# Optimization experiments

Hardware: AMD Instinct MI355X
Metric: run time of the kernel (lower is better)

The kernel has to match this reference:

```python
import jax, jax.numpy as jnp
import numpy as np

SMU_ALPHA = 0.25
SMU_MU = 1.0e6  # repo's act.SMU default: large mu -> smooth leaky-relu (max(x, alpha*x))

def smu(x):
    a = SMU_ALPHA
    return 0.5 * ((1.0 + a) * x + (1.0 - a) * x * jax.lax.erf(SMU_MU * (1.0 - a) * x))

def setup_inputs() -> dict:
    key = jax.random.key(0)
    ks = jax.random.split(key, 6)
    B, N, D = 8, 4096, 1024
    xavier = float(np.sqrt(6.0 / (D + D)))
    def lin_w(k):
        return jax.random.uniform(k, (D, D), jnp.float32, -xavier, xavier)
    return {
        "x": jax.random.normal(ks[0], (B, N, D), jnp.float32),
        "Wvr": lin_w(ks[1]), "bvr": jnp.zeros((D,), jnp.float32),
        "Wvi": lin_w(ks[2]), "bvi": jnp.zeros((D,), jnp.float32),
        "Wk": lin_w(ks[3]), "bk": jnp.zeros((D,), jnp.float32),
        "Wq": lin_w(ks[4]), "bq": jnp.zeros((D,), jnp.float32),
    }

def reference(x, Wvr, bvr, Wvi, bvi, Wk, bk, Wq, bq):
    # real input: real and imag branches both see x
    value_real = jnp.einsum('bnd,ed->bne', x, Wvr) + bvr
    value_imag = jnp.einsum('bnd,ed->bne', x, Wvi) + bvi
    # GLU: v_real * tanh(softplus(v_imag)); dropout disabled (p=0)
    value = value_real * jnp.tanh(jax.nn.softplus(value_imag))
    key_ = jnp.einsum('bnd,ed->bne', x, Wk) + bk
    query = jnp.einsum('bnd,ed->bne', x, Wq) + bq
    # L2 normalize along the sequence dim (dim=1)
    key_n = key_ / (jnp.linalg.norm(key_, axis=1, keepdims=True) + 1e-5)
    query_n = query / (jnp.linalg.norm(query, axis=1, keepdims=True) + 1e-5)
    feature_attn = smu(jnp.einsum('bnd,bne->bde', key_n, query_n))  # [B, D, D]
    return jnp.einsum('bnd,bde->bne', value, feature_attn)
```

## Files before the change

### kernel.cpp

```cpp
#include <hip/hip_runtime.h>
#include <math.h>

typedef __bf16 bf16x8 __attribute__((ext_vector_type(8)));
typedef float f32x4 __attribute__((ext_vector_type(4)));

#define MTOT 32768
#define DD   1024
#define NSEQ 4096
#define BB   8

__device__ __forceinline__ void async16(const void* gp, void* lp) {
  __builtin_amdgcn_global_load_lds(
      (__attribute__((address_space(1))) void*)(const_cast<void*>(gp)),
      (__attribute__((address_space(3))) void*)(lp), 16, 0, 0);
}

__device__ __forceinline__ unsigned short f2bf(float f) {
  union { float f; unsigned int u; } v; v.f = f;
  unsigned int r = v.u + 0x7fffu + ((v.u >> 16) & 1u);
  return (unsigned short)(r >> 16);
}
__device__ __forceinline__ float bf2f(unsigned short u) {
  union { unsigned int u; float f; } v; v.u = ((unsigned int)u) << 16; return v.f;
}

__device__ __forceinline__ unsigned lds_off(void* p) {
  return (unsigned)(unsigned long long)
      (__attribute__((address_space(3))) void*)p;
}
#define DSRI(dst, base, off) \
  asm volatile("ds_read_b128 %0, %1 offset:" #off : "=v"(dst) : "v"(base))

#define MFMA_ __builtin_amdgcn_mfma_f32_16x16x32_bf16

__global__ void cvt_bf16(const float* __restrict__ in, unsigned short* __restrict__ out, int n) {
  int i = (blockIdx.x * blockDim.x + threadIdx.x) * 8;
  if (i >= n) return;
  float4 a = *(const float4*)(in + i);
  float4 b = *(const float4*)(in + i + 4);
  ushort4 o0, o1;
  o0.x = f2bf(a.x); o0.y = f2bf(a.y); o0.z = f2bf(a.z); o0.w = f2bf(a.w);
  o1.x = f2bf(b.x); o1.y = f2bf(b.y); o1.z = f2bf(b.z); o1.w = f2bf(b.w);
  *(ushort4*)(out + i) = o0;
  *(ushort4*)(out + i + 4) = o1;
}

__global__ void cvt_w(const float* __restrict__ w0, const float* __restrict__ w1,
                      const float* __restrict__ w2, const float* __restrict__ w3,
                      unsigned short* __restrict__ out) {
  int z = blockIdx.y;
  const float* in = (z == 0) ? w0 : (z == 1) ? w1 : (z == 2) ? w2 : w3;
  int i = (blockIdx.x * blockDim.x + threadIdx.x) * 8;
  float4 a = *(const float4*)(in + i);
  float4 b = *(const float4*)(in + i + 4);
  ushort4 o0, o1;
  o0.x = f2bf(a.x); o0.y = f2bf(a.y); o0.z = f2bf(a.z); o0.w = f2bf(a.w);
  o1.x = f2bf(b.x); o1.y = f2bf(b.y); o1.z = f2bf(b.z); o1.w = f2bf(b.w);
  unsigned short* o = out + (size_t)z * DD * DD;
  *(ushort4*)(o + i) = o0;
  *(ushort4*)(o + i + 4) = o1;
}

template<int LDG>
__device__ __forceinline__ void stage_half(const unsigned short* __restrict__ g,
                                           int row0, int k0,
                                           unsigned short* lds, int tid) {
#pragma unroll
  for (int l = 0; l < 2; ++l) {
    int u = l * 512 + tid;
    int r = u >> 3;
    int sl = (u & 7) ^ (r & 7);
    async16(g + (size_t)(row0 + r) * LDG + k0 + sl * 8, (char*)lds + u * 16);
  }
}

__global__ __launch_bounds__(512, 2) void proj_all(
    const unsigned short* __restrict__ xb,
    const unsigned short* __restrict__ Wb,
    const float* __restrict__ bvr, const float* __restrict__ bvi,
    const float* __restrict__ bk,  const float* __restrict__ bq,
    unsigned short* __restrict__ oVr, unsigned short* __restrict__ oVi,
    unsigned short* __restrict__ Kt,  unsigned short* __restrict__ Qt,
    float* __restrict__ rnacc) {
  __shared__ __align__(16) unsigned short smem[65536];

  const int bx = blockIdx.x;
  const int swz = (bx & 7) * 64 + (bx >> 3);
  const int m0 = (swz >> 2) * 256;
  const int n0 = (swz & 3) * 256;
  const int z = blockIdx.z;
  const unsigned short* W = Wb + (size_t)z * DD * DD;
  const float* bias = (z == 0) ? bvr : (z == 1) ? bvi : (z == 2) ? bk : bq;

  const int tid = threadIdx.x;
  const int w = tid >> 6, lane = tid & 63;
  const int wr = w >> 2, wc = w & 3;
  const int lq = lane >> 4, lr = lane & 15;
  const int sx = lr & 7;
  const int arow0 = wr * 128 + lr;
  const int brow0 = wc * 64 + lr;

  f32x4 acc[8][4];
#pragma unroll
  for (int i = 0; i < 8; i++)
#pragma unroll
    for (int j = 0; j < 4; j++) acc[i][j] = (f32x4)(0.f);

  const int NT = 16;

  const unsigned sbase = lds_off(smem);
  const unsigned sw0 = (unsigned)((lq ^ sx) << 4);
  const unsigned sw1 = (unsigned)(((4 | lq) ^ sx) << 4);
  unsigned aA0 = sbase + arow0 * 128 + sw0;
  unsigned aA1 = sbase + arow0 * 128 + sw1;
  unsigned aB0 = sbase + 32768 + brow0 * 128 + sw0;
  unsigned aB1 = sbase + 32768 + brow0 * 128 + sw1;

  stage_half<1024>(xb, m0,       0,  smem,                     tid);
  stage_half<1024>(xb, m0 + 128, 0,  smem + 8192,              tid);
  stage_half<1024>(W,  n0,       0,  smem + 16384,             tid);
  stage_half<1024>(W,  n0 + 128, 0,  smem + 16384 + 8192,      tid);
  stage_half<1024>(W,  n0,       64, smem + 32768 + 16384,     tid);
  stage_half<1024>(W,  n0 + 128, 64, smem + 32768 + 16384 + 8192, tid);
  asm volatile("s_waitcnt vmcnt(4)" ::: "memory");
  __builtin_amdgcn_s_barrier();

  for (int t = 0; t < NT; ++t) {
    bf16x8 bfr[4][2], aL[4][2];
    DSRI(aL[0][0], aA0, 0);    DSRI(aL[0][1], aA1, 0);
    DSRI(bfr[0][0], aB0, 0);    DSRI(bfr[0][1], aB1, 0);
    DSRI(bfr[1][0], aB0, 2048); DSRI(bfr[1][1], aB1, 2048);
    DSRI(bfr[2][0], aB0, 4096); DSRI(bfr[2][1], aB1, 4096);
    DSRI(bfr[3][0], aB0, 6144); DSRI(bfr[3][1], aB1, 6144);
    DSRI(aL[1][0], aA0, 2048); DSRI(aL[1][1], aA1, 2048);
    DSRI(aL[2][0], aA0, 4096); DSRI(aL[2][1], aA1, 4096);
    DSRI(aL[3][0], aA0, 6144); DSRI(aL[3][1], aA1, 6144);
    if (t + 1 < NT) {
      stage_half<1024>(xb, m0,       (t + 1) * 64, smem + ((t + 1) & 1) * 32768, tid);
      stage_half<1024>(xb, m0 + 128, (t + 1) * 64, smem + ((t + 1) & 1) * 32768 + 8192, tid);
    }
    __builtin_amdgcn_s_barrier();
    asm volatile("s_waitcnt lgkmcnt(6)" ::: "memory");
    __builtin_amdgcn_sched_barrier(0);
    __builtin_amdgcn_s_setprio(1);
#pragma unroll
    for (int nj = 0; nj < 4; ++nj) {
      acc[0][nj] = MFMA_(aL[0][0], bfr[nj][0], acc[0][nj], 0, 0, 0);
      acc[0][nj] = MFMA_(aL[0][1], bfr[nj][1], acc[0][nj], 0, 0, 0);
    }
    asm volatile("s_waitcnt lgkmcnt(0)" ::: "memory");
    __builtin_amdgcn_sched_barrier(0);
#pragma unroll
    for (int mi = 1; mi < 4; ++mi)
#pragma unroll
      for (int nj = 0; nj < 4; ++nj) {
        acc[mi][nj] = MFMA_(aL[mi][0], bfr[nj][0], acc[mi][nj], 0, 0, 0);
        acc[mi][nj] = MFMA_(aL[mi][1], bfr[nj][1], acc[mi][nj], 0, 0, 0);
      }
    __builtin_amdgcn_s_setprio(0);
    __builtin_amdgcn_sched_barrier(0);
    __builtin_amdgcn_s_barrier();

    bf16x8 aH[4][2];
    DSRI(aH[0][0], aA0, 8192);  DSRI(aH[0][1], aA1, 8192);
    DSRI(aH[1][0], aA0, 10240); DSRI(aH[1][1], aA1, 10240);
    DSRI(aH[2][0], aA0, 12288); DSRI(aH[2][1], aA1, 12288);
    DSRI(aH[3][0], aA0, 14336); DSRI(aH[3][1], aA1, 14336);
    if (t + 2 < NT) {
      stage_half<1024>(W, n0,       (t + 2) * 64, smem + (t & 1) * 32768 + 16384, tid);
      stage_half<1024>(W, n0 + 128, (t + 2) * 64, smem + (t & 1) * 32768 + 16384 + 8192, tid);
    }
    __builtin_amdgcn_s_barrier();
    asm volatile("s_waitcnt lgkmcnt(4)" ::: "memory");
    __builtin_amdgcn_sched_barrier(0);
    __builtin_amdgcn_s_setprio(1);
#pragma unroll
    for (int mi = 0; mi < 2; ++mi)
#pragma unroll
      for (int nj = 0; nj < 4; ++nj) {
        acc[4 + mi][nj] = MFMA_(aH[mi][0], bfr[nj][0], acc[4 + mi][nj], 0, 0, 0);
        acc[4 + mi][nj] = MFMA_(aH[mi][1], bfr[nj][1], acc[4 + mi][nj], 0, 0, 0);
      }
    asm volatile("s_waitcnt lgkmcnt(0)" ::: "memory");
    __builtin_amdgcn_sched_barrier(0);
#pragma unroll
    for (int mi = 2; mi < 4; ++mi)
#pragma unroll
      for (int nj = 0; nj < 4; ++nj) {
        acc[4 + mi][nj] = MFMA_(aH[mi][0], bfr[nj][0], acc[4 + mi][nj], 0, 0, 0);
        acc[4 + mi][nj] = MFMA_(aH[mi][1], bfr[nj][1], acc[4 + mi][nj], 0, 0, 0);
      }
    __builtin_amdgcn_s_setprio(0);
    __builtin_amdgcn_sched_barrier(0);
    if (t < NT - 2)       asm volatile("s_waitcnt vmcnt(4)" ::: "memory");
    else if (t == NT - 2) asm volatile("s_waitcnt vmcnt(0)" ::: "memory");
    __builtin_amdgcn_s_barrier();

    aA0 ^= 65536u; aA1 ^= 65536u; aB0 ^= 65536u; aB1 ^= 65536u;
  }

  if (z < 2) {
    unsigned short* out = (z == 0) ? oVr : oVi;
#pragma unroll
    for (int nj = 0; nj < 4; ++nj) {
      int col = n0 + wc * 64 + nj * 16 + lr;
      float bv = bias[col];
#pragma unroll
      for (int mrep = 0; mrep < 8; ++mrep) {
        int rowb = m0 + wr * 128 + mrep * 16 + lq * 4;
#pragma unroll
        for (int r = 0; r < 4; ++r)
          out[(size_t)(rowb + r) * DD + col] = f2bf(acc[mrep][nj][r] + bv);
      }
    }
  } else {
    unsigned short* outp = (z == 2) ? Kt : Qt;
    const int which = z - 2;
    const int b = m0 >> 12;
    const int nbase = m0 & 4095;
    float* racc = rnacc + which * (BB * DD) + b * DD;
    unsigned short* T = smem;
    const int SP2 = 264;
#pragma unroll
    for (int ch = 0; ch < 2; ++ch) {
      if ((wc >> 1) == ch) {
#pragma unroll
        for (int nj = 0; nj < 4; ++nj) {
          int cloc = (wc & 1) * 64 + nj * 16 + lr;
          float bv = bias[n0 + ch * 128 + cloc];
#pragma unroll
          for (int mrep = 0; mrep < 8; ++mrep) {
            int rowb = wr * 128 + mrep * 16 + lq * 4;
            ushort4 pk;
            pk.x = f2bf(acc[mrep][nj][0] + bv); pk.y = f2bf(acc[mrep][nj][1] + bv);
            pk.z = f2bf(acc[mrep][nj][2] + bv); pk.w = f2bf(acc[mrep][nj][3] + bv);
            *(ushort4*)(T + cloc * SP2 + rowb) = pk;
          }
        }
      }
      __syncthreads();
#pragma unroll
      for (int p = 0; p < 8; ++p) {
        int dl = p * 16 + (tid >> 5);
        int nc = (tid & 31) * 8;
        ushort4 v0 = *(const ushort4*)(T + dl * SP2 + nc);
        ushort4 v1 = *(const ushort4*)(T + dl * SP2 + nc + 4);
        int d = n0 + ch * 128 + dl;
        *(ushort4*)(outp + (size_t)(b * DD + d) * NSEQ + nbase + nc)     = v0;
        *(ushort4*)(outp + (size_t)(b * DD + d) * NSEQ + nbase + nc + 4) = v1;
        float s = bf2f(v0.x)*bf2f(v0.x) + bf2f(v0.y)*bf2f(v0.y) + bf2f(v0.z)*bf2f(v0.z) + bf2f(v0.w)*bf2f(v0.w)
                + bf2f(v1.x)*bf2f(v1.x) + bf2f(v1.y)*bf2f(v1.y) + bf2f(v1.z)*bf2f(v1.z) + bf2f(v1.w)*bf2f(v1.w);
#pragma unroll
        for (int off = 1; off < 32; off <<= 1) s += __shfl_xor(s, off, 32);
        if ((tid & 31) == 0) atomicAdd(&racc[d], s);
      }
      __syncthreads();
    }
  }
}

__global__ void finalize_rn(float* __restrict__ rn) {
  int i = blockIdx.x * blockDim.x + threadIdx.x;
  rn[i] = 1.f / (sqrtf(rn[i]) + 1e-5f);
}

__global__ void glu(unsigned short* __restrict__ V, const unsigned short* __restrict__ Vi, int n) {
  int i = (blockIdx.x * blockDim.x + threadIdx.x) * 8;
  if (i >= n) return;
  ushort4 r0 = *(const ushort4*)(V + i);
  ushort4 r1 = *(const ushort4*)(V + i + 4);
  ushort4 i0 = *(const ushort4*)(Vi + i);
  ushort4 i1 = *(const ushort4*)(Vi + i + 4);
  unsigned short vr[8] = {r0.x, r0.y, r0.z, r0.w, r1.x, r1.y, r1.z, r1.w};
  unsigned short vi[8] = {i0.x, i0.y, i0.z, i0.w, i1.x, i1.y, i1.z, i1.w};
  unsigned short o[8];
#pragma unroll
  for (int k = 0; k < 8; k++) {
    float a = bf2f(vr[k]), b = bf2f(vi[k]);
    float g;
    if (b > 10.f) g = 1.f;
    else { float t = __expf(b); float u = t * (t + 2.f); g = u / (u + 2.f); }
    o[k] = f2bf(a * g);
  }
  *(ushort4*)(V + i)     = make_ushort4(o[0], o[1], o[2], o[3]);
  *(ushort4*)(V + i + 4) = make_ushort4(o[4], o[5], o[6], o[7]);
}

__global__ __launch_bounds__(512, 2) void attn_gemm(
    const unsigned short* __restrict__ Qt, const unsigned short* __restrict__ Kt,
    const float* __restrict__ rn, unsigned short* __restrict__ fat) {
  __shared__ __align__(16) unsigned short smem[57344];

  const int b = blockIdx.z;
  const int d0 = blockIdx.x * 128;
  const int e0 = blockIdx.y * 256;
  const unsigned short* A  = Qt + (size_t)b * DD * NSEQ;
  const unsigned short* Bm = Kt + (size_t)b * DD * NSEQ;
  unsigned short* out = fat + (size_t)b * DD * DD;

  const int tid = threadIdx.x;
  const int w = tid >> 6, lane = tid & 63;
  const int wr = w >> 1, wc = w & 1;
  const int lq = lane >> 4, lr = lane & 15;
  const int sx = lr & 7;
  const int arow0 = wr * 64 + lr;
  const int brow0 = wc * 64 + lr;

  f32x4 acc[4][4];
#pragma unroll
  for (int i = 0; i < 4; i++)
#pragma unroll
    for (int j = 0; j < 4; j++) acc[i][j] = (f32x4)(0.f);

  const int NT = 64;

  const unsigned sbase = lds_off(smem);
  const unsigned sw0 = (unsigned)((lq ^ sx) << 4);
  const unsigned sw1 = (unsigned)(((4 | lq) ^ sx) << 4);
// ... 63 lines not shown
      acc[3][nj] = MFMA_(aH[1][0], bfr[nj][0], acc[3][nj], 0, 0, 0);
      acc[3][nj] = MFMA_(aH[1][1], bfr[nj][1], acc[3][nj], 0, 0, 0);
    }
    __builtin_amdgcn_s_setprio(0);
    __builtin_amdgcn_sched_barrier(0);
    if (t < NT - 2)       asm volatile("s_waitcnt vmcnt(2)" ::: "memory");
    else if (t == NT - 2) asm volatile("s_waitcnt vmcnt(0)" ::: "memory");
    __builtin_amdgcn_s_barrier();

    aA0 ^= 65536u; aA1 ^= 65536u; aB0 ^= 65536u; aB1 ^= 65536u;
  }

#pragma unroll
  for (int nj = 0; nj < 4; ++nj) {
    int col = d0 + wc * 64 + nj * 16 + lr;
    float rk = rn[b * DD + col];
#pragma unroll
    for (int mi = 0; mi < 4; ++mi) {
      int rowb = e0 + wr * 64 + mi * 16 + lq * 4;
#pragma unroll
      for (int r = 0; r < 4; ++r) {
        float rq = rn[BB * DD + b * DD + rowb + r];
        float c = acc[mi][nj][r] * rq * rk;
        c = (c > 0.f) ? c : 0.25f * c;
        out[(size_t)(rowb + r) * DD + col] = f2bf(c);
      }
    }
  }
}

__global__ __launch_bounds__(512, 2) void out_gemm(
    const unsigned short* __restrict__ V, const unsigned short* __restrict__ fat,
    float* __restrict__ out) {
  __shared__ __align__(16) unsigned short smem[65536];

  const int bx = blockIdx.x;
  const int swz = (bx & 7) * 64 + (bx >> 3);
  const int m0 = (swz >> 2) * 256;
  const int e0 = (swz & 3) * 256;
  const int b = m0 >> 12;
  const unsigned short* Bm = fat + (size_t)b * DD * DD;

  const int tid = threadIdx.x;
  const int w = tid >> 6, lane = tid & 63;
  const int wr = w >> 2, wc = w & 3;
  const int lq = lane >> 4, lr = lane & 15;
  const int sx = lr & 7;
  const int arow0 = wr * 128 + lr;
  const int brow0 = wc * 64 + lr;

  f32x4 acc[8][4];
#pragma unroll
  for (int i = 0; i < 8; i++)
#pragma unroll
    for (int j = 0; j < 4; j++) acc[i][j] = (f32x4)(0.f);

  const int NT = 16;

  const unsigned sbase = lds_off(smem);
  const unsigned sw0 = (unsigned)((lq ^ sx) << 4);
  const unsigned sw1 = (unsigned)(((4 | lq) ^ sx) << 4);
  unsigned aA0 = sbase + arow0 * 128 + sw0;
  unsigned aA1 = sbase + arow0 * 128 + sw1;
  unsigned aB0 = sbase + 32768 + brow0 * 128 + sw0;
  unsigned aB1 = sbase + 32768 + brow0 * 128 + sw1;

  stage_half<1024>(V,  m0,       0,  smem,                        tid);
  stage_half<1024>(V,  m0 + 128, 0,  smem + 8192,                 tid);
  stage_half<1024>(Bm, e0,       0,  smem + 16384,                tid);
  stage_half<1024>(Bm, e0 + 128, 0,  smem + 16384 + 8192,         tid);
  stage_half<1024>(Bm, e0,       64, smem + 32768 + 16384,        tid);
  stage_half<1024>(Bm, e0 + 128, 64, smem + 32768 + 16384 + 8192, tid);
  asm volatile("s_waitcnt vmcnt(4)" ::: "memory");
  __builtin_amdgcn_s_barrier();

  for (int t = 0; t < NT; ++t) {
    bf16x8 bfr[4][2], aL[4][2];
    DSRI(aL[0][0], aA0, 0);    DSRI(aL[0][1], aA1, 0);
    DSRI(bfr[0][0], aB0, 0);    DSRI(bfr[0][1], aB1, 0);
    DSRI(bfr[1][0], aB0, 2048); DSRI(bfr[1][1], aB1, 2048);
    DSRI(bfr[2][0], aB0, 4096); DSRI(bfr[2][1], aB1, 4096);
    DSRI(bfr[3][0], aB0, 6144); DSRI(bfr[3][1], aB1, 6144);
    DSRI(aL[1][0], aA0, 2048); DSRI(aL[1][1], aA1, 2048);
    DSRI(aL[2][0], aA0, 4096); DSRI(aL[2][1], aA1, 4096);
    DSRI(aL[3][0], aA0, 6144); DSRI(aL[3][1], aA1, 6144);
    if (t + 1 < NT) {
      stage_half<1024>(V, m0,       (t + 1) * 64, smem + ((t + 1) & 1) * 32768, tid);
      stage_half<1024>(V, m0 + 128, (t + 1) * 64, smem + ((t + 1) & 1) * 32768 + 8192, tid);
    }
    __builtin_amdgcn_s_barrier();
    asm volatile("s_waitcnt lgkmcnt(6)" ::: "memory");
    __builtin_amdgcn_sched_barrier(0);
    __builtin_amdgcn_s_setprio(1);
#pragma unroll
    for (int nj = 0; nj < 4; ++nj) {
      acc[0][nj] = MFMA_(aL[0][0], bfr[nj][0], acc[0][nj], 0, 0, 0);
      acc[0][nj] = MFMA_(aL[0][1], bfr[nj][1], acc[0][nj], 0, 0, 0);
    }
    asm volatile("s_waitcnt lgkmcnt(0)" ::: "memory");
    __builtin_amdgcn_sched_barrier(0);
#pragma unroll
    for (int mi = 1; mi < 4; ++mi)
#pragma unroll
      for (int nj = 0; nj < 4; ++nj) {
        acc[mi][nj] = MFMA_(aL[mi][0], bfr[nj][0], acc[mi][nj], 0, 0, 0);
        acc[mi][nj] = MFMA_(aL[mi][1], bfr[nj][1], acc[mi][nj], 0, 0, 0);
      }
    __builtin_amdgcn_s_setprio(0);
    __builtin_amdgcn_sched_barrier(0);
    __builtin_amdgcn_s_barrier();

    bf16x8 aH[4][2];
    DSRI(aH[0][0], aA0, 8192);  DSRI(aH[0][1], aA1, 8192);
    DSRI(aH[1][0], aA0, 10240); DSRI(aH[1][1], aA1, 10240);
    DSRI(aH[2][0], aA0, 12288); DSRI(aH[2][1], aA1, 12288);
    DSRI(aH[3][0], aA0, 14336); DSRI(aH[3][1], aA1, 14336);
    if (t + 2 < NT) {
      stage_half<1024>(Bm, e0,       (t + 2) * 64, smem + (t & 1) * 32768 + 16384, tid);
      stage_half<1024>(Bm, e0 + 128, (t + 2) * 64, smem + (t & 1) * 32768 + 16384 + 8192, tid);
    }
    __builtin_amdgcn_s_barrier();
    asm volatile("s_waitcnt lgkmcnt(4)" ::: "memory");
    __builtin_amdgcn_sched_barrier(0);
    __builtin_amdgcn_s_setprio(1);
#pragma unroll
    for (int mi = 0; mi < 2; ++mi)
#pragma unroll
      for (int nj = 0; nj < 4; ++nj) {
        acc[4 + mi][nj] = MFMA_(aH[mi][0], bfr[nj][0], acc[4 + mi][nj], 0, 0, 0);
        acc[4 + mi][nj] = MFMA_(aH[mi][1], bfr[nj][1], acc[4 + mi][nj], 0, 0, 0);
      }
    asm volatile("s_waitcnt lgkmcnt(0)" ::: "memory");
    __builtin_amdgcn_sched_barrier(0);
#pragma unroll
    for (int mi = 2; mi < 4; ++mi)
#pragma unroll
      for (int nj = 0; nj < 4; ++nj) {
        acc[4 + mi][nj] = MFMA_(aH[mi][0], bfr[nj][0], acc[4 + mi][nj], 0, 0, 0);
        acc[4 + mi][nj] = MFMA_(aH[mi][1], bfr[nj][1], acc[4 + mi][nj], 0, 0, 0);
      }
    __builtin_amdgcn_s_setprio(0);
    __builtin_amdgcn_sched_barrier(0);
    if (t < NT - 2)       asm volatile("s_waitcnt vmcnt(4)" ::: "memory");
    else if (t == NT - 2) asm volatile("s_waitcnt vmcnt(0)" ::: "memory");
    __builtin_amdgcn_s_barrier();

    aA0 ^= 65536u; aA1 ^= 65536u; aB0 ^= 65536u; aB1 ^= 65536u;
  }

#pragma unroll
  for (int nj = 0; nj < 4; ++nj) {
    int col = e0 + wc * 64 + nj * 16 + lr;
#pragma unroll
    for (int mrep = 0; mrep < 8; ++mrep) {
      int rowb = m0 + wr * 128 + mrep * 16 + lq * 4;
#pragma unroll
      for (int r = 0; r < 4; ++r)
        out[(size_t)(rowb + r) * DD + col] = acc[mrep][nj][r];
    }
  }
}

extern "C" void kernel_launch(void* const* d_in, const int* in_sizes, int n_in,
                              void* d_out, int out_size, void* d_ws, size_t ws_size,
                              hipStream_t stream) {
  const float* x   = (const float*)d_in[0];
  const float* Wvr = (const float*)d_in[1];
  const float* bvr = (const float*)d_in[2];
  const float* Wvi = (const float*)d_in[3];
  const float* bvi = (const float*)d_in[4];
  const float* Wk  = (const float*)d_in[5];
  const float* bk  = (const float*)d_in[6];
  const float* Wq  = (const float*)d_in[7];
  const float* bq  = (const float*)d_in[8];
  float* out = (float*)d_out;

  char* p = (char*)d_ws;
  unsigned short* xb  = (unsigned short*)p; p += (size_t)MTOT * DD * 2;
  unsigned short* Wb  = (unsigned short*)p; p += 4ull * DD * DD * 2;
  unsigned short* Kt  = (unsigned short*)p; p += (size_t)BB * DD * NSEQ * 2;
  unsigned short* Qt  = (unsigned short*)p; p += (size_t)BB * DD * NSEQ * 2;
  unsigned short* Vb  = (unsigned short*)p; p += (size_t)MTOT * DD * 2;
  unsigned short* fat = (unsigned short*)p; p += (size_t)BB * DD * DD * 2;
  float* rn = (float*)p; p += 2ull * BB * DD * sizeof(float);

  unsigned short* ViBuf = (unsigned short*)d_out;

  int nx = MTOT * DD;
  int nw = DD * DD;
  cvt_bf16<<<nx / 8 / 256, 256, 0, stream>>>(x, xb, nx);
  cvt_w<<<dim3(nw / 8 / 256, 4), 256, 0, stream>>>(Wvr, Wvi, Wk, Wq, Wb);
  hipMemsetAsync(rn, 0, 2ull * BB * DD * sizeof(float), stream);

  proj_all<<<dim3(512, 1, 4), 512, 0, stream>>>(
      xb, Wb, bvr, bvi, bk, bq, Vb, ViBuf, Kt, Qt, rn);

  glu<<<nx / 8 / 256, 256, 0, stream>>>(Vb, ViBuf, nx);
  finalize_rn<<<2 * BB * DD / 256, 256, 0, stream>>>(rn);

  attn_gemm<<<dim3(DD / 128, DD / 256, BB), 512, 0, stream>>>(Qt, Kt, rn, fat);
  out_gemm<<<dim3(512), 512, 0, stream>>>(Vb, fat, out);
}
```

Before: 729.9 us.

## Restructure projection and output GEMMs into a triple-buffered K=32 register-pipelined loop

Both bf16 GEMM kernels (projection and output) now step through K in tiles of 32 instead of 64. Shared-memory tiles move from a double buffer to a triple-buffered ring with one barrier per step. A and B fragments are double-buffered in registers so the next step's LDS reads overlap the current MFMAs. The XOR swizzle on shared memory is dropped, which may bring LDS bank conflicts back. Register pressure rises, and the number of barrier-separated steps doubles.

```diff
diff --git a/kernel.cpp b/kernel.cpp
--- a/kernel.cpp
+++ b/kernel.cpp
@@ -62,6 +62,19 @@
 }
 
 template<int LDG>
+__device__ __forceinline__ void stage32(const unsigned short* __restrict__ g,
+                                        int row0, int k0,
+                                        unsigned short* lds, int tid) {
+#pragma unroll
+  for (int l = 0; l < 2; ++l) {
+    int u = l * 512 + tid;
+    int r = u >> 2;
+    int c = u & 3;
+    async16(g + (size_t)(row0 + r) * LDG + k0 + c * 8, (char*)lds + u * 16);
+  }
+}
+
+template<int LDG>
 __device__ __forceinline__ void stage_half(const unsigned short* __restrict__ g,
                                            int row0, int k0,
                                            unsigned short* lds, int tid) {
@@ -82,7 +95,7 @@
     unsigned short* __restrict__ oVr, unsigned short* __restrict__ oVi,
     unsigned short* __restrict__ Kt,  unsigned short* __restrict__ Qt,
     float* __restrict__ rnacc) {
-  __shared__ __align__(16) unsigned short smem[65536];
+  __shared__ __align__(16) unsigned short smem[49152];
 
   const int bx = blockIdx.x;
   const int swz = (bx & 7) * 64 + (bx >> 3);
@@ -96,7 +109,6 @@
   const int w = tid >> 6, lane = tid & 63;
   const int wr = w >> 2, wc = w & 3;
   const int lq = lane >> 4, lr = lane & 15;
-  const int sx = lr & 7;
   const int arow0 = wr * 128 + lr;
   const int brow0 = wc * 64 + lr;
 
@@ -106,98 +118,89 @@
 #pragma unroll
     for (int j = 0; j < 4; j++) acc[i][j] = (f32x4)(0.f);
 
-  const int NT = 16;
+  const int NT = 32;
 
   const unsigned sbase = lds_off(smem);
-  const unsigned sw0 = (unsigned)((lq ^ sx) << 4);
-  const unsigned sw1 = (unsigned)(((4 | lq) ^ sx) << 4);
-  unsigned aA0 = sbase + arow0 * 128 + sw0;
-  unsigned aA1 = sbase + arow0 * 128 + sw1;
-  unsigned aB0 = sbase + 32768 + brow0 * 128 + sw0;
-  unsigned aB1 = sbase + 32768 + brow0 * 128 + sw1;
-
-  stage_half<1024>(xb, m0,       0,  smem,                     tid);
-  stage_half<1024>(xb, m0 + 128, 0,  smem + 8192,              tid);
-  stage_half<1024>(W,  n0,       0,  smem + 16384,             tid);
-  stage_half<1024>(W,  n0 + 128, 0,  smem + 16384 + 8192,      tid);
-  stage_half<1024>(W,  n0,       64, smem + 32768 + 16384,     tid);
-  stage_half<1024>(W,  n0 + 128, 64, smem + 32768 + 16384 + 8192, tid);
+  unsigned aA[3], aB[3];
+#pragma unroll
+  for (int i = 0; i < 3; ++i) {
+    aA[i] = sbase + i * 32768u + (unsigned)(arow0 * 64 + lq * 16);
+    aB[i] = sbase + i * 32768u + 32768u / 2u + (unsigned)(brow0 * 64 + lq * 16);
+  }
+
+  bf16x8 A1[4], B0[2][4], A2[2][4];
+
+  stage32<1024>(xb, m0, 0,  smem,                tid);
+  stage32<1024>(W,  n0, 0,  smem + 8192,         tid);
+  stage32<1024>(xb, m0, 32, smem + 16384,        tid);
+  stage32<1024>(W,  n0, 32, smem + 16384 + 8192, tid);
   asm volatile("s_waitcnt vmcnt(4)" ::: "memory");
   __builtin_amdgcn_s_barrier();
 
-  for (int t = 0; t < NT; ++t) {
-    bf16x8 bfr[4][2], aL[4][2];
-    DSRI(aL[0][0], aA0, 0);    DSRI(aL[0][1], aA1, 0);
-    DSRI(bfr[0][0], aB0, 0);    DSRI(bfr[0][1], aB1, 0);
-    DSRI(bfr[1][0], aB0, 2048); DSRI(bfr[1][1], aB1, 2048);
-    DSRI(bfr[2][0], aB0, 4096); DSRI(bfr[2][1], aB1, 4096);
-    DSRI(bfr[3][0], aB0, 6144); DSRI(bfr[3][1], aB1, 6144);
-    DSRI(aL[1][0], aA0, 2048); DSRI(aL[1][1], aA1, 2048);
-    DSRI(aL[2][0], aA0, 4096); DSRI(aL[2][1], aA1, 4096);
-    DSRI(aL[3][0], aA0, 6144); DSRI(aL[3][1], aA1, 6144);
-    if (t + 1 < NT) {
-      stage_half<1024>(xb, m0,       (t + 1) * 64, smem + ((t + 1) & 1) * 32768, tid);
-      stage_half<1024>(xb, m0 + 128, (t + 1) * 64, smem + ((t + 1) & 1) * 32768 + 8192, tid);
-    }
+  DSRI(A1[0],    aA[0], 0);    DSRI(A1[1],    aA[0], 1024);
+  DSRI(A1[2],    aA[0], 2048); DSRI(A1[3],    aA[0], 3072);
+  DSRI(B0[0][0], aB[0], 0);    DSRI(B0[0][1], aB[0], 1024);
+  DSRI(B0[0][2], aB[0], 2048); DSRI(B0[0][3], aB[0], 3072);
+  DSRI(A2[0][0], aA[0], 4096); DSRI(A2[0][1], aA[0], 5120);
+  DSRI(A2[0][2], aA[0], 6144); DSRI(A2[0][3], aA[0], 7168);
+  asm volatile("s_waitcnt lgkmcnt(4)" ::: "memory");
+  __builtin_amdgcn_sched_barrier(0);
+  __builtin_amdgcn_s_setprio(1);
+#pragma unroll
+  for (int mi = 0; mi < 4; ++mi)
+#pragma unroll
+    for (int nj = 0; nj < 4; ++nj)
+      acc[mi][nj] = MFMA_(A1[mi], B0[0][nj], acc[mi][nj], 0, 0, 0);
+  __builtin_amdgcn_s_setprio(0);
+  __builtin_amdgcn_sched_barrier(0);
+  asm volatile("s_waitcnt vmcnt(0)" ::: "memory");
+  __builtin_amdgcn_s_barrier();
+
+#pragma unroll
+  for (int k = 0; k < NT - 1; ++k) {
+    const int cs = k & 1, ns = (k + 1) & 1;
+    const unsigned rA = aA[(k + 1) % 3], rB = aB[(k + 1) % 3];
+    DSRI(A1[0],     rA, 0);    DSRI(A1[1],     rA, 1024);
+    DSRI(A1[2],     rA, 2048); DSRI(A1[3],     rA, 3072);
+    DSRI(B0[ns][0], rB, 0);    DSRI(B0[ns][1], rB, 1024);
+    DSRI(B0[ns][2], rB, 2048); DSRI(B0[ns][3], rB, 3072);
+    DSRI(A2[ns][0], rA, 4096); DSRI(A2[ns][1], rA, 5120);
+    DSRI(A2[ns][2], rA, 6144); DSRI(A2[ns][3], rA, 7168);
+    if (k + 2 < NT) {
+      unsigned short* d = smem + ((k + 2) % 3) * 16384;
+      stage32<1024>(xb, m0, (k + 2) * 32, d,        tid);
+      stage32<1024>(W,  n0, (k + 2) * 32, d + 8192, tid);
+    }
+    asm volatile("s_waitcnt lgkmcnt(12)" ::: "memory");
+    __builtin_amdgcn_sched_barrier(0);
+    __builtin_amdgcn_s_setprio(1);
+#pragma unroll
+    for (int mi = 0; mi < 4; ++mi)
+#pragma unroll
+      for (int nj = 0; nj < 4; ++nj)
+        acc[4 + mi][nj] = MFMA_(A2[cs][mi], B0[cs][nj], acc[4 + mi][nj], 0, 0, 0);
+    __builtin_amdgcn_s_setprio(0);
+    __builtin_amdgcn_sched_barrier(0);
+    asm volatile("s_waitcnt lgkmcnt(4)" ::: "memory");
+    __builtin_amdgcn_sched_barrier(0);
+    __builtin_amdgcn_s_setprio(1);
+#pragma unroll
+    for (int mi = 0; mi < 4; ++mi)
+#pragma unroll
+      for (int nj = 0; nj < 4; ++nj)
+        acc[mi][nj] = MFMA_(A1[mi], B0[ns][nj], acc[mi][nj], 0, 0, 0);
+    __builtin_amdgcn_s_setprio(0);
+    __builtin_amdgcn_sched_barrier(0);
+    asm volatile("s_waitcnt vmcnt(0)" ::: "memory");
     __builtin_amdgcn_s_barrier();
-    asm volatile("s_waitcnt lgkmcnt(6)" ::: "memory");
-    __builtin_amdgcn_sched_barrier(0);
-    __builtin_amdgcn_s_setprio(1);
-#pragma unroll
-    for (int nj = 0; nj < 4; ++nj) {
-      acc[0][nj] = MFMA_(aL[0][0], bfr[nj][0], acc[0][nj], 0, 0, 0);
-      acc[0][nj] = MFMA_(aL[0][1], bfr[nj][1], acc[0][nj], 0, 0, 0);
-    }
-    asm volatile("s_waitcnt lgkmcnt(0)" ::: "memory");
-    __builtin_amdgcn_sched_barrier(0);
-#pragma unroll
-    for (int mi = 1; mi < 4; ++mi)
-#pragma unroll
-      for (int nj = 0; nj < 4; ++nj) {
-        acc[mi][nj] = MFMA_(aL[mi][0], bfr[nj][0], acc[mi][nj], 0, 0, 0);
-        acc[mi][nj] = MFMA_(aL[mi][1], bfr[nj][1], acc[mi][nj], 0, 0, 0);
-      }
-    __builtin_amdgcn_s_setprio(0);
-    __builtin_amdgcn_sched_barrier(0);
-    __builtin_amdgcn_s_barrier();
-
-    bf16x8 aH[4][2];
-    DSRI(aH[0][0], aA0, 8192);  DSRI(aH[0][1], aA1, 8192);
-    DSRI(aH[1][0], aA0, 10240); DSRI(aH[1][1], aA1, 10240);
-    DSRI(aH[2][0], aA0, 12288); DSRI(aH[2][1], aA1, 12288);
-    DSRI(aH[3][0], aA0, 14336); DSRI(aH[3][1], aA1, 14336);
-    if (t + 2 < NT) {
-      stage_half<1024>(W, n0,       (t + 2) * 64, smem + (t & 1) * 32768 + 16384, tid);
-      stage_half<1024>(W, n0 + 128, (t + 2) * 64, smem + (t & 1) * 32768 + 16384 + 8192, tid);
-    }
-    __builtin_amdgcn_s_barrier();
-    asm volatile("s_waitcnt lgkmcnt(4)" ::: "memory");
-    __builtin_amdgcn_sched_barrier(0);
-    __builtin_amdgcn_s_setprio(1);
-#pragma unroll
-    for (int mi = 0; mi < 2; ++mi)
-#pragma unroll
-      for (int nj = 0; nj < 4; ++nj) {
-        acc[4 + mi][nj] = MFMA_(aH[mi][0], bfr[nj][0], acc[4 + mi][nj], 0, 0, 0);
-        acc[4 + mi][nj] = MFMA_(aH[mi][1], bfr[nj][1], acc[4 + mi][nj], 0, 0, 0);
-      }
-    asm volatile("s_waitcnt lgkmcnt(0)" ::: "memory");
-    __builtin_amdgcn_sched_barrier(0);
-#pragma unroll
-    for (int mi = 2; mi < 4; ++mi)
-#pragma unroll
-      for (int nj = 0; nj < 4; ++nj) {
-        acc[4 + mi][nj] = MFMA_(aH[mi][0], bfr[nj][0], acc[4 + mi][nj], 0, 0, 0);
-        acc[4 + mi][nj] = MFMA_(aH[mi][1], bfr[nj][1], acc[4 + mi][nj], 0, 0, 0);
-      }
-    __builtin_amdgcn_s_setprio(0);
-    __builtin_amdgcn_sched_barrier(0);
-    if (t < NT - 2)       asm volatile("s_waitcnt vmcnt(4)" ::: "memory");
-    else if (t == NT - 2) asm volatile("s_waitcnt vmcnt(0)" ::: "memory");
-    __builtin_amdgcn_s_barrier();
-
-    aA0 ^= 65536u; aA1 ^= 65536u; aB0 ^= 65536u; aB1 ^= 65536u;
-  }
+  }
+  asm volatile("s_waitcnt lgkmcnt(0)" ::: "memory");
+  __builtin_amdgcn_sched_barrier(0);
+#pragma unroll
+  for (int mi = 0; mi < 4; ++mi)
+#pragma unroll
+    for (int nj = 0; nj < 4; ++nj)
+      acc[4 + mi][nj] = MFMA_(A2[1][mi], B0[1][nj], acc[4 + mi][nj], 0, 0, 0);
 
   if (z < 2) {
     unsigned short* out = (z == 0) ? oVr : oVi;
@@ -214,6 +217,7 @@
       }
     }
   } else {
+    __syncthreads();
     unsigned short* outp = (z == 2) ? Kt : Qt;
     const int which = z - 2;
     const int b = m0 >> 12;
@@ -413,7 +417,7 @@
 __global__ __launch_bounds__(512, 2) void out_gemm(
     const unsigned short* __restrict__ V, const unsigned short* __restrict__ fat,
     float* __restrict__ out) {
-  __shared__ __align__(16) unsigned short smem[65536];
+  __shared__ __align__(16) unsigned short smem[49152];
 
   const int bx = blockIdx.x;
   const int swz = (bx & 7) * 64 + (bx >> 3);
@@ -426,7 +430,6 @@
   const int w = tid >> 6, lane = tid & 63;
   const int wr = w >> 2, wc = w & 3;
   const int lq = lane >> 4, lr = lane & 15;
-  const int sx = lr & 7;
   const int arow0 = wr * 128 + lr;
   const int brow0 = wc * 64 + lr;
 
@@ -436,98 +439,89 @@
 #pragma unroll
     for (int j = 0; j < 4; j++) acc[i][j] = (f32x4)(0.f);
 
-  const int NT = 16;
+  const int NT = 32;
 
   const unsigned sbase = lds_off(smem);
-  const unsigned sw0 = (unsigned)((lq ^ sx) << 4);
-  const unsigned sw1 = (unsigned)(((4 | lq) ^ sx) << 4);
-  unsigned aA0 = sbase + arow0 * 128 + sw0;
-  unsigned aA1 = sbase + arow0 * 128 + sw1;
-  unsigned aB0 = sbase + 32768 + brow0 * 128 + sw0;
-  unsigned aB1 = sbase + 32768 + brow0 * 128 + sw1;
-
-  stage_half<1024>(V,  m0,       0,  smem,                        tid);
-  stage_half<1024>(V,  m0 + 128, 0,  smem + 8192,                 tid);
-  stage_half<1024>(Bm, e0,       0,  smem + 16384,                tid);
-  stage_half<1024>(Bm, e0 + 128, 0,  smem + 16384 + 8192,         tid);
-  stage_half<1024>(Bm, e0,       64, smem + 32768 + 16384,        tid);
-  stage_half<1024>(Bm, e0 + 128, 64, smem + 32768 + 16384 + 8192, tid);
+  unsigned aA[3], aB[3];
+#pragma unroll
+  for (int i = 0; i < 3; ++i) {
+    aA[i] = sbase + i * 32768u + (unsigned)(arow0 * 64 + lq * 16);
+    aB[i] = sbase + i * 32768u + 16384u + (unsigned)(brow0 * 64 + lq * 16);
+  }
+
+  bf16x8 A1[4], B0[2][4], A2[2][4];
+
+  stage32<1024>(V,  m0, 0,  smem,                tid);
+  stage32<1024>(Bm, e0, 0,  smem + 8192,         tid);
+  stage32<1024>(V,  m0, 32, smem + 16384,        tid);
+  stage32<1024>(Bm, e0, 32, smem + 16384 + 8192, tid);
   asm volatile("s_waitcnt vmcnt(4)" ::: "memory");
   __builtin_amdgcn_s_barrier();
 
-  for (int t = 0; t < NT; ++t) {
-    bf16x8 bfr[4][2], aL[4][2];
-    DSRI(aL[0][0], aA0, 0);    DSRI(aL[0][1], aA1, 0);
-    DSRI(bfr[0][0], aB0, 0);    DSRI(bfr[0][1], aB1, 0);
-    DSRI(bfr[1][0], aB0, 2048); DSRI(bfr[1][1], aB1, 2048);
-    DSRI(bfr[2][0], aB0, 4096); DSRI(bfr[2][1], aB1, 4096);
-    DSRI(bfr[3][0], aB0, 6144); DSRI(bfr[3][1], aB1, 6144);
-    DSRI(aL[1][0], aA0, 2048); DSRI(aL[1][1], aA1, 2048);
-    DSRI(aL[2][0], aA0, 4096); DSRI(aL[2][1], aA1, 4096);
-    DSRI(aL[3][0], aA0, 6144); DSRI(aL[3][1], aA1, 6144);
-    if (t + 1 < NT) {
-      stage_half<1024>(V, m0,       (t + 1) * 64, smem + ((t + 1) & 1) * 32768, tid);
-      stage_half<1024>(V, m0 + 128, (t + 1) * 64, smem + ((t + 1) & 1) * 32768 + 8192, tid);
-    }
+  DSRI(A1[0],    aA[0], 0);    DSRI(A1[1],    aA[0], 1024);
+  DSRI(A1[2],    aA[0], 2048); DSRI(A1[3],    aA[0], 3072);
+  DSRI(B0[0][0], aB[0], 0);    DSRI(B0[0][1], aB[0], 1024);
+  DSRI(B0[0][2], aB[0], 2048); DSRI(B0[0][3], aB[0], 3072);
+  DSRI(A2[0][0], aA[0], 4096); DSRI(A2[0][1], aA[0], 5120);
+  DSRI(A2[0][2], aA[0], 6144); DSRI(A2[0][3], aA[0], 7168);
+  asm volatile("s_waitcnt lgkmcnt(4)" ::: "memory");
+  __builtin_amdgcn_sched_barrier(0);
+  __builtin_amdgcn_s_setprio(1);
+#pragma unroll
+  for (int mi = 0; mi < 4; ++mi)
+#pragma unroll
+    for (int nj = 0; nj < 4; ++nj)
+      acc[mi][nj] = MFMA_(A1[mi], B0[0][nj], acc[mi][nj], 0, 0, 0);
+  __builtin_amdgcn_s_setprio(0);
+  __builtin_amdgcn_sched_barrier(0);
+  asm volatile("s_waitcnt vmcnt(0)" ::: "memory");
+  __builtin_amdgcn_s_barrier();
+
+#pragma unroll
+  for (int k = 0; k < NT - 1; ++k) {
+    const int cs = k & 1, ns = (k + 1) & 1;
+    const unsigned rA = aA[(k + 1) % 3], rB = aB[(k + 1) % 3];
+    DSRI(A1[0],     rA, 0);    DSRI(A1[1],     rA, 1024);
+    DSRI(A1[2],     rA, 2048); DSRI(A1[3],     rA, 3072);
+    DSRI(B0[ns][0], rB, 0);    DSRI(B0[ns][1], rB, 1024);
+    DSRI(B0[ns][2], rB, 2048); DSRI(B0[ns][3], rB, 3072);
+    DSRI(A2[ns][0], rA, 4096); DSRI(A2[ns][1], rA, 5120);
+    DSRI(A2[ns][2], rA, 6144); DSRI(A2[ns][3], rA, 7168);
+    if (k + 2 < NT) {
+      unsigned short* d = smem + ((k + 2) % 3) * 16384;
+      stage32<1024>(V,  m0, (k + 2) * 32, d,        tid);
+      stage32<1024>(Bm, e0, (k + 2) * 32, d + 8192, tid);
+    }
+    asm volatile("s_waitcnt lgkmcnt(12)" ::: "memory");
+    __builtin_amdgcn_sched_barrier(0);
+    __builtin_amdgcn_s_setprio(1);
+#pragma unroll
+    for (int mi = 0; mi < 4; ++mi)
+#pragma unroll
+      for (int nj = 0; nj < 4; ++nj)
+        acc[4 + mi][nj] = MFMA_(A2[cs][mi], B0[cs][nj], acc[4 + mi][nj], 0, 0, 0);
+    __builtin_amdgcn_s_setprio(0);
+    __builtin_amdgcn_sched_barrier(0);
+    asm volatile("s_waitcnt lgkmcnt(4)" ::: "memory");
+    __builtin_amdgcn_sched_barrier(0);
+    __builtin_amdgcn_s_setprio(1);
+#pragma unroll
+    for (int mi = 0; mi < 4; ++mi)
+#pragma unroll
+      for (int nj = 0; nj < 4; ++nj)
+        acc[mi][nj] = MFMA_(A1[mi], B0[ns][nj], acc[mi][nj], 0, 0, 0);
+    __builtin_amdgcn_s_setprio(0);
+    __builtin_amdgcn_sched_barrier(0);
+    asm volatile("s_waitcnt vmcnt(0)" ::: "memory");
     __builtin_amdgcn_s_barrier();
-    asm volatile("s_waitcnt lgkmcnt(6)" ::: "memory");
-    __builtin_amdgcn_sched_barrier(0);
-    __builtin_amdgcn_s_setprio(1);
-#pragma unroll
-    for (int nj = 0; nj < 4; ++nj) {
-      acc[0][nj] = MFMA_(aL[0][0], bfr[nj][0], acc[0][nj], 0, 0, 0);
-      acc[0][nj] = MFMA_(aL[0][1], bfr[nj][1], acc[0][nj], 0, 0, 0);
-    }
-    asm volatile("s_waitcnt lgkmcnt(0)" ::: "memory");
-    __builtin_amdgcn_sched_barrier(0);
-#pragma unroll
-    for (int mi = 1; mi < 4; ++mi)
-#pragma unroll
-      for (int nj = 0; nj < 4; ++nj) {
-        acc[mi][nj] = MFMA_(aL[mi][0], bfr[nj][0], acc[mi][nj], 0, 0, 0);
-        acc[mi][nj] = MFMA_(aL[mi][1], bfr[nj][1], acc[mi][nj], 0, 0, 0);
-      }
-    __builtin_amdgcn_s_setprio(0);
-    __builtin_amdgcn_sched_barrier(0);
-    __builtin_amdgcn_s_barrier();
-
-    bf16x8 aH[4][2];
-    DSRI(aH[0][0], aA0, 8192);  DSRI(aH[0][1], aA1, 8192);
-    DSRI(aH[1][0], aA0, 10240); DSRI(aH[1][1], aA1, 10240);
-    DSRI(aH[2][0], aA0, 12288); DSRI(aH[2][1], aA1, 12288);
-    DSRI(aH[3][0], aA0, 14336); DSRI(aH[3][1], aA1, 14336);
-    if (t + 2 < NT) {
-      stage_half<1024>(Bm, e0,       (t + 2) * 64, smem + (t & 1) * 32768 + 16384, tid);
-      stage_half<1024>(Bm, e0 + 128, (t + 2) * 64, smem + (t & 1) * 32768 + 16384 + 8192, tid);
-    }
-    __builtin_amdgcn_s_barrier();
-    asm volatile("s_waitcnt lgkmcnt(4)" ::: "memory");
-    __builtin_amdgcn_sched_barrier(0);
-    __builtin_amdgcn_s_setprio(1);
-#pragma unroll
-    for (int mi = 0; mi < 2; ++mi)
-#pragma unroll
-      for (int nj = 0; nj < 4; ++nj) {
-        acc[4 + mi][nj] = MFMA_(aH[mi][0], bfr[nj][0], acc[4 + mi][nj], 0, 0, 0);
-        acc[4 + mi][nj] = MFMA_(aH[mi][1], bfr[nj][1], acc[4 + mi][nj], 0, 0, 0);
-      }
-    asm volatile("s_waitcnt lgkmcnt(0)" ::: "memory");
-    __builtin_amdgcn_sched_barrier(0);
-#pragma unroll
-    for (int mi = 2; mi < 4; ++mi)
-#pragma unroll
-      for (int nj = 0; nj < 4; ++nj) {
-        acc[4 + mi][nj] = MFMA_(aH[mi][0], bfr[nj][0], acc[4 + mi][nj], 0, 0, 0);
-        acc[4 + mi][nj] = MFMA_(aH[mi][1], bfr[nj][1], acc[4 + mi][nj], 0, 0, 0);
-      }
-    __builtin_amdgcn_s_setprio(0);
-    __builtin_amdgcn_sched_barrier(0);
-    if (t < NT - 2)       asm volatile("s_waitcnt vmcnt(4)" ::: "memory");
-    else if (t == NT - 2) asm volatile("s_waitcnt vmcnt(0)" ::: "memory");
-    __builtin_amdgcn_s_barrier();
-
-    aA0 ^= 65536u; aA1 ^= 65536u; aB0 ^= 65536u; aB1 ^= 65536u;
-  }
+  }
+  asm volatile("s_waitcnt lgkmcnt(0)" ::: "memory");
+  __builtin_amdgcn_sched_barrier(0);
+#pragma unroll
+  for (int mi = 0; mi < 4; ++mi)
+#pragma unroll
+    for (int nj = 0; nj < 4; ++nj)
+      acc[4 + mi][nj] = MFMA_(A2[1][mi], B0[1][nj], acc[4 + mi][nj], 0, 0, 0);
 
 #pragma unroll
   for (int nj = 0; nj < 4; ++nj) {
```

Result: slower. 761.2 us (+4.3%).

## Fuse GLU gating into value projection epilogue with two-pass z=0 blocks

Applied to the files above, without the earlier changes.

Value blocks now compute the imaginary projection first, keeping its bias-added bf16 result packed in registers. They then compute the real projection and apply the tanh(softplus) gate in the epilogue before writing the gated value. This removes the separate GLU kernel and the intermediate imaginary-value buffer round-trip through global memory. The cost is uneven per-block work (z=0 blocks do two GEMM passes) and extra register pressure from the packed buffers.

```diff
diff --git a/kernel.cpp b/kernel.cpp
--- a/kernel.cpp
+++ b/kernel.cpp
@@ -22,6 +22,9 @@
 }
 __device__ __forceinline__ float bf2f(unsigned short u) {
   union { unsigned int u; float f; } v; v.u = ((unsigned int)u) << 16; return v.f;
+}
+__device__ __forceinline__ unsigned pk2(float a, float b) {
+  return (unsigned)f2bf(a) | ((unsigned)f2bf(b) << 16);
 }
 
 __device__ __forceinline__ unsigned lds_off(void* p) {
@@ -79,7 +82,7 @@
     const unsigned short* __restrict__ Wb,
     const float* __restrict__ bvr, const float* __restrict__ bvi,
     const float* __restrict__ bk,  const float* __restrict__ bq,
-    unsigned short* __restrict__ oVr, unsigned short* __restrict__ oVi,
+    unsigned short* __restrict__ oV,
     unsigned short* __restrict__ Kt,  unsigned short* __restrict__ Qt,
     float* __restrict__ rnacc) {
   __shared__ __align__(16) unsigned short smem[65536];
@@ -89,8 +92,6 @@
   const int m0 = (swz >> 2) * 256;
   const int n0 = (swz & 3) * 256;
   const int z = blockIdx.z;
-  const unsigned short* W = Wb + (size_t)z * DD * DD;
-  const float* bias = (z == 0) ? bvr : (z == 1) ? bvi : (z == 2) ? bk : bq;
 
   const int tid = threadIdx.x;
   const int w = tid >> 6, lane = tid & 63;
@@ -106,6 +107,8 @@
 #pragma unroll
     for (int j = 0; j < 4; j++) acc[i][j] = (f32x4)(0.f);
 
+  unsigned pkx[8][4], pky[8][4];
+
   const int NT = 16;
 
   const unsigned sbase = lds_off(smem);
@@ -116,106 +119,134 @@
   unsigned aB0 = sbase + 32768 + brow0 * 128 + sw0;
   unsigned aB1 = sbase + 32768 + brow0 * 128 + sw1;
 
-  stage_half<1024>(xb, m0,       0,  smem,                     tid);
-  stage_half<1024>(xb, m0 + 128, 0,  smem + 8192,              tid);
-  stage_half<1024>(W,  n0,       0,  smem + 16384,             tid);
-  stage_half<1024>(W,  n0 + 128, 0,  smem + 16384 + 8192,      tid);
-  stage_half<1024>(W,  n0,       64, smem + 32768 + 16384,     tid);
-  stage_half<1024>(W,  n0 + 128, 64, smem + 32768 + 16384 + 8192, tid);
-  asm volatile("s_waitcnt vmcnt(4)" ::: "memory");
-  __builtin_amdgcn_s_barrier();
-
-  for (int t = 0; t < NT; ++t) {
-    bf16x8 bfr[4][2], aL[4][2];
-    DSRI(aL[0][0], aA0, 0);    DSRI(aL[0][1], aA1, 0);
-    DSRI(bfr[0][0], aB0, 0);    DSRI(bfr[0][1], aB1, 0);
-    DSRI(bfr[1][0], aB0, 2048); DSRI(bfr[1][1], aB1, 2048);
-    DSRI(bfr[2][0], aB0, 4096); DSRI(bfr[2][1], aB1, 4096);
-    DSRI(bfr[3][0], aB0, 6144); DSRI(bfr[3][1], aB1, 6144);
-    DSRI(aL[1][0], aA0, 2048); DSRI(aL[1][1], aA1, 2048);
-    DSRI(aL[2][0], aA0, 4096); DSRI(aL[2][1], aA1, 4096);
-    DSRI(aL[3][0], aA0, 6144); DSRI(aL[3][1], aA1, 6144);
-    if (t + 1 < NT) {
-      stage_half<1024>(xb, m0,       (t + 1) * 64, smem + ((t + 1) & 1) * 32768, tid);
-      stage_half<1024>(xb, m0 + 128, (t + 1) * 64, smem + ((t + 1) & 1) * 32768 + 8192, tid);
-    }
-    __builtin_amdgcn_s_barrier();
-    asm volatile("s_waitcnt lgkmcnt(6)" ::: "memory");
-    __builtin_amdgcn_sched_barrier(0);
-    __builtin_amdgcn_s_setprio(1);
-#pragma unroll
-    for (int nj = 0; nj < 4; ++nj) {
-      acc[0][nj] = MFMA_(aL[0][0], bfr[nj][0], acc[0][nj], 0, 0, 0);
-      acc[0][nj] = MFMA_(aL[0][1], bfr[nj][1], acc[0][nj], 0, 0, 0);
-    }
-    asm volatile("s_waitcnt lgkmcnt(0)" ::: "memory");
-    __builtin_amdgcn_sched_barrier(0);
-#pragma unroll
-    for (int mi = 1; mi < 4; ++mi)
+  const int npass = (z == 0) ? 2 : 1;
+  for (int pass = 0; pass < npass; ++pass) {
+    const unsigned short* W =
+        (z == 0) ? (Wb + (size_t)(pass == 0 ? 1 : 0) * DD * DD)
+                 : (Wb + (size_t)(z + 1) * DD * DD);
+
+    stage_half<1024>(xb, m0,       0,  smem,                     tid);
+    stage_half<1024>(xb, m0 + 128, 0,  smem + 8192,              tid);
+    stage_half<1024>(W,  n0,       0,  smem + 16384,             tid);
+    stage_half<1024>(W,  n0 + 128, 0,  smem + 16384 + 8192,      tid);
+    stage_half<1024>(W,  n0,       64, smem + 32768 + 16384,     tid);
+    stage_half<1024>(W,  n0 + 128, 64, smem + 32768 + 16384 + 8192, tid);
+    asm volatile("s_waitcnt vmcnt(4)" ::: "memory");
+    __builtin_amdgcn_s_barrier();
+
+    for (int t = 0; t < NT; ++t) {
+      bf16x8 bfr[4][2], aL[4][2];
+      DSRI(aL[0][0], aA0, 0);    DSRI(aL[0][1], aA1, 0);
+      DSRI(bfr[0][0], aB0, 0);    DSRI(bfr[0][1], aB1, 0);
+      DSRI(bfr[1][0], aB0, 2048); DSRI(bfr[1][1], aB1, 2048);
+      DSRI(bfr[2][0], aB0, 4096); DSRI(bfr[2][1], aB1, 4096);
+      DSRI(bfr[3][0], aB0, 6144); DSRI(bfr[3][1], aB1, 6144);
+      DSRI(aL[1][0], aA0, 2048); DSRI(aL[1][1], aA1, 2048);
+      DSRI(aL[2][0], aA0, 4096); DSRI(aL[2][1], aA1, 4096);
+      DSRI(aL[3][0], aA0, 6144); DSRI(aL[3][1], aA1, 6144);
+      if (t + 1 < NT) {
+        stage_half<1024>(xb, m0,       (t + 1) * 64, smem + ((t + 1) & 1) * 32768, tid);
+        stage_half<1024>(xb, m0 + 128, (t + 1) * 64, smem + ((t + 1) & 1) * 32768 + 8192, tid);
+      }
+      __builtin_amdgcn_s_barrier();
+      asm volatile("s_waitcnt lgkmcnt(6)" ::: "memory");
+      __builtin_amdgcn_sched_barrier(0);
+      __builtin_amdgcn_s_setprio(1);
 #pragma unroll
       for (int nj = 0; nj < 4; ++nj) {
-        acc[mi][nj] = MFMA_(aL[mi][0], bfr[nj][0], acc[mi][nj], 0, 0, 0);
-        acc[mi][nj] = MFMA_(aL[mi][1], bfr[nj][1], acc[mi][nj], 0, 0, 0);
-      }
-    __builtin_amdgcn_s_setprio(0);
-    __builtin_amdgcn_sched_barrier(0);
-    __builtin_amdgcn_s_barrier();
-
-    bf16x8 aH[4][2];
-    DSRI(aH[0][0], aA0, 8192);  DSRI(aH[0][1], aA1, 8192);
-    DSRI(aH[1][0], aA0, 10240); DSRI(aH[1][1], aA1, 10240);
-    DSRI(aH[2][0], aA0, 12288); DSRI(aH[2][1], aA1, 12288);
-    DSRI(aH[3][0], aA0, 14336); DSRI(aH[3][1], aA1, 14336);
-    if (t + 2 < NT) {
-      stage_half<1024>(W, n0,       (t + 2) * 64, smem + (t & 1) * 32768 + 16384, tid);
-      stage_half<1024>(W, n0 + 128, (t + 2) * 64, smem + (t & 1) * 32768 + 16384 + 8192, tid);
-    }
-    __builtin_amdgcn_s_barrier();
-    asm volatile("s_waitcnt lgkmcnt(4)" ::: "memory");
-    __builtin_amdgcn_sched_barrier(0);
-    __builtin_amdgcn_s_setprio(1);
-#pragma unroll
-    for (int mi = 0; mi < 2; ++mi)
+        acc[0][nj] = MFMA_(aL[0][0], bfr[nj][0], acc[0][nj], 0, 0, 0);
+        acc[0][nj] = MFMA_(aL[0][1], bfr[nj][1], acc[0][nj], 0, 0, 0);
+      }
+      asm volatile("s_waitcnt lgkmcnt(0)" ::: "memory");
+      __builtin_amdgcn_sched_barrier(0);
+#pragma unroll
+      for (int mi = 1; mi < 4; ++mi)
+#pragma unroll
+        for (int nj = 0; nj < 4; ++nj) {
+          acc[mi][nj] = MFMA_(aL[mi][0], bfr[nj][0], acc[mi][nj], 0, 0, 0);
+          acc[mi][nj] = MFMA_(aL[mi][1], bfr[nj][1], acc[mi][nj], 0, 0, 0);
+        }
+      __builtin_amdgcn_s_setprio(0);
+      __builtin_amdgcn_sched_barrier(0);
+      __builtin_amdgcn_s_barrier();
+
+      bf16x8 aH[4][2];
+      DSRI(aH[0][0], aA0, 8192);  DSRI(aH[0][1], aA1, 8192);
+      DSRI(aH[1][0], aA0, 10240); DSRI(aH[1][1], aA1, 10240);
+      DSRI(aH[2][0], aA0, 12288); DSRI(aH[2][1], aA1, 12288);
+      DSRI(aH[3][0], aA0, 14336); DSRI(aH[3][1], aA1, 14336);
+      if (t + 2 < NT) {
+        stage_half<1024>(W, n0,       (t + 2) * 64, smem + (t & 1) * 32768 + 16384, tid);
+        stage_half<1024>(W, n0 + 128, (t + 2) * 64, smem + (t & 1) * 32768 + 16384 + 8192, tid);
+      }
+      __builtin_amdgcn_s_barrier();
+      asm volatile("s_waitcnt lgkmcnt(4)" ::: "memory");
+      __builtin_amdgcn_sched_barrier(0);
+      __builtin_amdgcn_s_setprio(1);
+#pragma unroll
+      for (int mi = 0; mi < 2; ++mi)
+#pragma unroll
+        for (int nj = 0; nj < 4; ++nj) {
+          acc[4 + mi][nj] = MFMA_(aH[mi][0], bfr[nj][0], acc[4 + mi][nj], 0, 0, 0);
+          acc[4 + mi][nj] = MFMA_(aH[mi][1], bfr[nj][1], acc[4 + mi][nj], 0, 0, 0);
+        }
+      asm volatile("s_waitcnt lgkmcnt(0)" ::: "memory");
+      __builtin_amdgcn_sched_barrier(0);
+#pragma unroll
+      for (int mi = 2; mi < 4; ++mi)
+#pragma unroll
+        for (int nj = 0; nj < 4; ++nj) {
+          acc[4 + mi][nj] = MFMA_(aH[mi][0], bfr[nj][0], acc[4 + mi][nj], 0, 0, 0);
+          acc[4 + mi][nj] = MFMA_(aH[mi][1], bfr[nj][1], acc[4 + mi][nj], 0, 0, 0);
+        }
+      __builtin_amdgcn_s_setprio(0);
+      __builtin_amdgcn_sched_barrier(0);
+      if (t < NT - 2)       asm volatile("s_waitcnt vmcnt(4)" ::: "memory");
+      else if (t == NT - 2) asm volatile("s_waitcnt vmcnt(0)" ::: "memory");
+      __builtin_amdgcn_s_barrier();
+
+      aA0 ^= 65536u; aA1 ^= 65536u; aB0 ^= 65536u; aB1 ^= 65536u;
+    }
+
+    if (z == 0 && pass == 0) {
 #pragma unroll
       for (int nj = 0; nj < 4; ++nj) {
-        acc[4 + mi][nj] = MFMA_(aH[mi][0], bfr[nj][0], acc[4 + mi][nj], 0, 0, 0);
-        acc[4 + mi][nj] = MFMA_(aH[mi][1], bfr[nj][1], acc[4 + mi][nj], 0, 0, 0);
-      }
-    asm volatile("s_waitcnt lgkmcnt(0)" ::: "memory");
-    __builtin_amdgcn_sched_barrier(0);
-#pragma unroll
-    for (int mi = 2; mi < 4; ++mi)
-#pragma unroll
-      for (int nj = 0; nj < 4; ++nj) {
-        acc[4 + mi][nj] = MFMA_(aH[mi][0], bfr[nj][0], acc[4 + mi][nj], 0, 0, 0);
-        acc[4 + mi][nj] = MFMA_(aH[mi][1], bfr[nj][1], acc[4 + mi][nj], 0, 0, 0);
-      }
-    __builtin_amdgcn_s_setprio(0);
-    __builtin_amdgcn_sched_barrier(0);
-    if (t < NT - 2)       asm volatile("s_waitcnt vmcnt(4)" ::: "memory");
-    else if (t == NT - 2) asm volatile("s_waitcnt vmcnt(0)" ::: "memory");
-    __builtin_amdgcn_s_barrier();
-
-    aA0 ^= 65536u; aA1 ^= 65536u; aB0 ^= 65536u; aB1 ^= 65536u;
-  }
-
-  if (z < 2) {
-    unsigned short* out = (z == 0) ? oVr : oVi;
+        int col = n0 + wc * 64 + nj * 16 + lr;
+        float bv = bvi[col];
+#pragma unroll
+        for (int mrep = 0; mrep < 8; ++mrep) {
+          pkx[mrep][nj] = pk2(acc[mrep][nj][0] + bv, acc[mrep][nj][1] + bv);
+          pky[mrep][nj] = pk2(acc[mrep][nj][2] + bv, acc[mrep][nj][3] + bv);
+          acc[mrep][nj] = (f32x4)(0.f);
+        }
+      }
+    }
+  }
+
+  if (z == 0) {
 #pragma unroll
     for (int nj = 0; nj < 4; ++nj) {
       int col = n0 + wc * 64 + nj * 16 + lr;
-      float bv = bias[col];
+      float bv = bvr[col];
 #pragma unroll
       for (int mrep = 0; mrep < 8; ++mrep) {
         int rowb = m0 + wr * 128 + mrep * 16 + lq * 4;
 #pragma unroll
-        for (int r = 0; r < 4; ++r)
-          out[(size_t)(rowb + r) * DD + col] = f2bf(acc[mrep][nj][r] + bv);
+        for (int r = 0; r < 4; ++r) {
+          float vr = bf2f(f2bf(acc[mrep][nj][r] + bv));
+          unsigned p = (r < 2) ? pkx[mrep][nj] : pky[mrep][nj];
+          float vi = bf2f((unsigned short)((r & 1) ? (p >> 16) : (p & 0xffffu)));
+          float g;
+          if (vi > 10.f) g = 1.f;
+          else { float tt = __expf(vi); float u = tt * (tt + 2.f); g = u / (u + 2.f); }
+          oV[(size_t)(rowb + r) * DD + col] = f2bf(vr * g);
+        }
       }
     }
   } else {
-    unsigned short* outp = (z == 2) ? Kt : Qt;
-    const int which = z - 2;
+    const float* bias = (z == 1) ? bk : bq;
+    unsigned short* outp = (z == 1) ? Kt : Qt;
+    const int which = z - 1;
     const int b = m0 >> 12;
     const int nbase = m0 & 4095;
     float* racc = rnacc + which * (BB * DD) + b * DD;
@@ -262,28 +293,6 @@
 __global__ void finalize_rn(float* __restrict__ rn) {
   int i = blockIdx.x * blockDim.x + threadIdx.x;
   rn[i] = 1.f / (sqrtf(rn[i]) + 1e-5f);
-}
-
-__global__ void glu(unsigned short* __restrict__ V, const unsigned short* __restrict__ Vi, int n) {
-  int i = (blockIdx.x * blockDim.x + threadIdx.x) * 8;
-  if (i >= n) return;
-  ushort4 r0 = *(const ushort4*)(V + i);
-  ushort4 r1 = *(const ushort4*)(V + i + 4);
-  ushort4 i0 = *(const ushort4*)(Vi + i);
-  ushort4 i1 = *(const ushort4*)(Vi + i + 4);
-  unsigned short vr[8] = {r0.x, r0.y, r0.z, r0.w, r1.x, r1.y, r1.z, r1.w};
-  unsigned short vi[8] = {i0.x, i0.y, i0.z, i0.w, i1.x, i1.y, i1.z, i1.w};
-  unsigned short o[8];
-#pragma unroll
-  for (int k = 0; k < 8; k++) {
-    float a = bf2f(vr[k]), b = bf2f(vi[k]);
-    float g;
-    if (b > 10.f) g = 1.f;
-    else { float t = __expf(b); float u = t * (t + 2.f); g = u / (u + 2.f); }
-    o[k] = f2bf(a * g);
-  }
-  *(ushort4*)(V + i)     = make_ushort4(o[0], o[1], o[2], o[3]);
-  *(ushort4*)(V + i + 4) = make_ushort4(o[4], o[5], o[6], o[7]);
 }
 
 __global__ __launch_bounds__(512, 2) void attn_gemm(
@@ -565,18 +574,15 @@
   unsigned short* fat = (unsigned short*)p; p += (size_t)BB * DD * DD * 2;
   float* rn = (float*)p; p += 2ull * BB * DD * sizeof(float);
 
-  unsigned short* ViBuf = (unsigned short*)d_out;
-
   int nx = MTOT * DD;
   int nw = DD * DD;
   cvt_bf16<<<nx / 8 / 256, 256, 0, stream>>>(x, xb, nx);
   cvt_w<<<dim3(nw / 8 / 256, 4), 256, 0, stream>>>(Wvr, Wvi, Wk, Wq, Wb);
   hipMemsetAsync(rn, 0, 2ull * BB * DD * sizeof(float), stream);
 
-  proj_all<<<dim3(512, 1, 4), 512, 0, stream>>>(
-      xb, Wb, bvr, bvi, bk, bq, Vb, ViBuf, Kt, Qt, rn);
-
-  glu<<<nx / 8 / 256, 256, 0, stream>>>(Vb, ViBuf, nx);
+  proj_all<<<dim3(512, 1, 3), 512, 0, stream>>>(
+      xb, Wb, bvr, bvi, bk, bq, Vb, Kt, Qt, rn);
+
   finalize_rn<<<2 * BB * DD / 256, 256, 0, stream>>>(rn);
 
   attn_gemm<<<dim3(DD / 128, DD / 256, BB), 512, 0, stream>>>(Qt, Kt, rn, fat);
```

After: 717.0 us. Within noise of the previous version (-1.8%).
